# Kernel optimization log

Measured on AMD Instinct MI355X. Metric: run time of the kernel, lower is better.

Reference implementation:

```python
import jax, jax.numpy as jnp
import numpy as np

N_EMBD = 1024
N_HEADS = 16
HEAD_DIM = N_EMBD // N_HEADS


def setup_inputs() -> dict:
    key = jax.random.key(0)
    ks = jax.random.split(key, 5)
    s = 0.02
    return {
        "x": jax.random.normal(ks[0], (4, 2048, N_EMBD), dtype=jnp.float32),
        "w_attn": jax.random.normal(ks[1], (N_EMBD, 3 * N_EMBD), dtype=jnp.float32) * s,
        "b_attn": jnp.zeros((3 * N_EMBD,), dtype=jnp.float32),
        "w_proj": jax.random.normal(ks[2], (N_EMBD, N_EMBD), dtype=jnp.float32) * s,
        "b_proj": jnp.zeros((N_EMBD,), dtype=jnp.float32),
    }


def reference(x, w_attn, b_attn, w_proj, b_proj):
    B, T, C = x.shape
    H, D = N_HEADS, HEAD_DIM
    qkv = x @ w_attn + b_attn                      # [B,T,3C]
    q, k, v = jnp.split(qkv, 3, axis=-1)
    q = q.reshape(B, T, H, D).transpose(0, 2, 1, 3)  # [B,H,T,D]
    k = k.reshape(B, T, H, D).transpose(0, 2, 1, 3)
    v = v.reshape(B, T, H, D).transpose(0, 2, 1, 3)
    # Faithful to source bug: divide by d**(-0.5) == multiply by sqrt(d)
    scale = jnp.asarray(D, x.dtype) ** 0.5
    scores = jnp.einsum("bhqd,bhkd->bhqk", q, k) * scale  # [B,H,T,T]
    causal = jnp.tril(jnp.ones((T, T), dtype=bool))
    scores = jnp.where(causal[None, None], scores, -jnp.inf)
    attn = jax.nn.softmax(scores, axis=-1)
    y = jnp.einsum("bhqk,bhkd->bhqd", attn, v)     # [B,H,T,D]
    y = y.transpose(0, 2, 1, 3).reshape(B, T, C)
    return y @ w_proj + b_proj
```

## Files before the change

### kernel.cpp

```cpp
#include <hip/hip_runtime.h>
#include <cmath>

#define BB 4
#define TT 2048
#define CC 1024
#define HH 16
#define DD 64
#define MM (BB*TT)

typedef _Float16 f16x8 __attribute__((ext_vector_type(8)));
typedef _Float16 f16x4 __attribute__((ext_vector_type(4)));
typedef _Float16 f16x2 __attribute__((ext_vector_type(2)));
typedef float f32x4 __attribute__((ext_vector_type(4)));
typedef unsigned short ushort_t;

#define MFMA16(a,b,c) __builtin_amdgcn_mfma_f32_16x16x16f16(a,b,c,0,0,0)

__device__ __forceinline__ unsigned short f2h(float f) {
    _Float16 h = (_Float16)f;
    return __builtin_bit_cast(unsigned short, h);
}

__device__ __forceinline__ f16x2 cvt_pk(float a, float b) {
    return __builtin_bit_cast(f16x2, __builtin_amdgcn_cvt_pkrtz(a, b));
}

__device__ __forceinline__ void gld16(const void* gsrc, void* ldst) {
    void* g = const_cast<void*>(gsrc);
    __builtin_amdgcn_global_load_lds(
        (__attribute__((address_space(1))) void*)g,
        (__attribute__((address_space(3))) void*)ldst,
        16, 0, 0);
}

__global__ __launch_bounds__(256)
void cvt4_kernel(const float* __restrict__ in, ushort_t* __restrict__ out, long n4) {
    long i = (long)blockIdx.x * blockDim.x + threadIdx.x;
    if (i >= n4) return;
    float4 v = ((const float4*)in)[i];
    ushort4 o;
    o.x = f2h(v.x); o.y = f2h(v.y); o.z = f2h(v.z); o.w = f2h(v.w);
    ((ushort4*)out)[i] = o;
}

__global__ __launch_bounds__(256)
void trcvt_kernel(const float* __restrict__ in, ushort_t* __restrict__ out,
                  int K, int N) {
    __shared__ float T[32][33];
    const int tx = threadIdx.x & 31;
    const int ty = threadIdx.x >> 5;
    const int n0 = blockIdx.x * 32;
    const int k0 = blockIdx.y * 32;
    #pragma unroll
    for (int i = 0; i < 4; ++i)
        T[ty + i * 8][tx] = in[(size_t)(k0 + ty + i * 8) * N + n0 + tx];
    __syncthreads();
    #pragma unroll
    for (int i = 0; i < 4; ++i)
        out[(size_t)(n0 + ty + i * 8) * K + k0 + tx] = f2h(T[tx][ty + i * 8]);
}

template<int N, bool QKV>
__global__ __launch_bounds__(256)
void hgemm_kernel(const ushort_t* __restrict__ A, const ushort_t* __restrict__ Bt,
                  const float* __restrict__ bias, float* __restrict__ out,
                  ushort_t* __restrict__ qh, ushort_t* __restrict__ kh,
                  ushort_t* __restrict__ vh)
{
    const int K = 1024;
    __shared__ ushort_t As[128 * 32];
    __shared__ ushort_t Bs[128 * 32];

    const int tid  = threadIdx.x;
    const int lane = tid & 63;
    const int wave = tid >> 6;
    const int wm   = (wave & 1) * 64;
    const int wn   = (wave >> 1) * 64;
    const int m0   = blockIdx.y * 128;
    const int n0   = blockIdx.x * 128;
    const int lrow = lane & 15;
    const int quad = lane >> 4;

    const int u0 = wave * 64 + lane;
    const int u1 = u0 + 256;
    const size_t gA0 = (size_t)(m0 + (u0 >> 2)) * K + (u0 & 3) * 8;
    const size_t gA1 = (size_t)(m0 + (u1 >> 2)) * K + (u1 & 3) * 8;
    const size_t gB0 = (size_t)(n0 + (u0 >> 2)) * K + (u0 & 3) * 8;
    const size_t gB1 = (size_t)(n0 + (u1 >> 2)) * K + (u1 & 3) * 8;
    ushort_t* ldsA0 = &As[(wave * 64) * 8];
    ushort_t* ldsA1 = &As[(256 + wave * 64) * 8];
    ushort_t* ldsB0 = &Bs[(wave * 64) * 8];
    ushort_t* ldsB1 = &Bs[(256 + wave * 64) * 8];

    f32x4 acc[4][4];
    const f32x4 z = {0.f, 0.f, 0.f, 0.f};
    #pragma unroll
    for (int mt = 0; mt < 4; ++mt)
        #pragma unroll
        for (int nt = 0; nt < 4; ++nt)
            acc[mt][nt] = z;

    for (int kk = 0; kk < K; kk += 32) {
        gld16(&A[gA0 + kk],  ldsA0);
        gld16(&A[gA1 + kk],  ldsA1);
        gld16(&Bt[gB0 + kk], ldsB0);
        gld16(&Bt[gB1 + kk], ldsB1);
        __syncthreads();

        f16x8 af[4], bf[4];
        #pragma unroll
        for (int mt = 0; mt < 4; ++mt)
            af[mt] = *(const f16x8*)&As[(wm + mt * 16 + lrow) * 32 + quad * 8];
        #pragma unroll
        for (int nt = 0; nt < 4; ++nt)
            bf[nt] = *(const f16x8*)&Bs[(wn + nt * 16 + lrow) * 32 + quad * 8];
        #pragma unroll
        for (int mt = 0; mt < 4; ++mt)
            #pragma unroll
            for (int nt = 0; nt < 4; ++nt)
                acc[mt][nt] = __builtin_amdgcn_mfma_f32_16x16x32_f16(
                    af[mt], bf[nt], acc[mt][nt], 0, 0, 0);
        __syncthreads();
    }

    #pragma unroll
    for (int mt = 0; mt < 4; ++mt) {
        const int rbase = m0 + wm + mt * 16 + quad * 4;
        #pragma unroll
        for (int nt = 0; nt < 4; ++nt) {
            const int col = n0 + wn + nt * 16 + lrow;
            const float bv = bias[col];
            if (QKV) {
                const int which = col >> 10;
                const int c = col & 1023;
                const int h = c >> 6, d = c & 63;
                const int b = rbase >> 11, t0 = rbase & 2047;
                if (which == 2) {
                    ushort4 pk;
                    pk.x = f2h(acc[mt][nt][0] + bv);
                    pk.y = f2h(acc[mt][nt][1] + bv);
                    pk.z = f2h(acc[mt][nt][2] + bv);
                    pk.w = f2h(acc[mt][nt][3] + bv);
                    *(ushort4*)&vh[(((size_t)b * HH + h) * DD + d) * TT + t0] = pk;
                } else {
                    ushort_t* dst = which ? kh : qh;
                    const float sc = which ? 1.0f : 8.0f * 1.44269504088896f;
                    #pragma unroll
                    for (int r = 0; r < 4; ++r)
                        dst[(((size_t)b * HH + h) * TT + t0 + r) * DD + d] =
                            f2h((acc[mt][nt][r] + bv) * sc);
                }
            } else {
                #pragma unroll
                for (int r = 0; r < 4; ++r)
                    out[(size_t)(rbase + r) * N + col] = acc[mt][nt][r] + bv;
            }
        }
    }
}

__global__ __launch_bounds__(256, 4)
void attn_mfma_kernel(const ushort_t* __restrict__ qh, const ushort_t* __restrict__ kh,
                      const ushort_t* __restrict__ vh, ushort_t* __restrict__ yh)
{
    __shared__ ushort_t Ks[2][64 * 72];
    __shared__ ushort_t Vs[2][64 * 72];

    const int pr   = blockIdx.x;
    const int bh   = blockIdx.y;
    const int qtA  = 31 - pr;
    const int qtB  = pr;
    const int tid  = threadIdx.x;
    const int lane = tid & 63;
    const int w    = tid >> 6;
    const int lrow = lane & 15;
    const int quad = lane >> 4;

    const ushort_t* qbase = qh + (size_t)bh * TT * DD;
    const ushort_t* kbase = kh + (size_t)bh * TT * DD;
    const ushort_t* vbase = vh + (size_t)bh * DD * TT;
    const int b = bh >> 4, h = bh & 15;

    const int ur = tid >> 3;
    const int uc = (tid & 7) * 8;

    int q0w = qtA * 64 + w * 16;
    f16x8 aq0 = *(const f16x8*)&qbase[(size_t)(q0w + lrow) * DD + quad * 8];
    f16x8 aq1 = *(const f16x8*)&qbase[(size_t)(q0w + lrow) * DD + 32 + quad * 8];

    const f32x4 z = {0.f, 0.f, 0.f, 0.f};
    f32x4 o[4] = {z, z, z, z};
    float mi = -1e30f, li = 0.f;

    uint4 kr0 = *(const uint4*)&kbase[(size_t)ur * DD + uc];
    uint4 kr1 = *(const uint4*)&kbase[(size_t)(ur + 32) * DD + uc];
    uint4 vr0 = *(const uint4*)&vbase[(size_t)ur * TT + uc];
    uint4 vr1 = *(const uint4*)&vbase[(size_t)(ur + 32) * TT + uc];

    *(uint4*)&Ks[0][(ur)      * 72 + uc] = kr0;
    *(uint4*)&Ks[0][(ur + 32) * 72 + uc] = kr1;
    *(uint4*)&Vs[0][(ur)      * 72 + uc] = vr0;
    *(uint4*)&Vs[0][(ur + 32) * 72 + uc] = vr1;
    {
        const int nkt = (1 <= qtA) ? 1 : 0;
        const int nb  = nkt * 64;
        kr0 = *(const uint4*)&kbase[(size_t)(nb + ur) * DD + uc];
        kr1 = *(const uint4*)&kbase[(size_t)(nb + ur + 32) * DD + uc];
        vr0 = *(const uint4*)&vbase[(size_t)ur * TT + nb + uc];
        vr1 = *(const uint4*)&vbase[(size_t)(ur + 32) * TT + nb + uc];
    }
    __syncthreads();

    for (int i = 0; i <= 32; ++i) {
        const int cur = i & 1;
        if (i == qtA + 1) {
            #pragma unroll
            for (int r = 0; r < 4; ++r) {
                const float inv = 1.0f / __shfl(li, quad * 4 + r, 64);
                const int t = q0w + quad * 4 + r;
                #pragma unroll
                for (int dt = 0; dt < 4; ++dt)
                    yh[((size_t)b * TT + t) * CC + h * 64 + dt * 16 + lrow] =
                        f2h(o[dt][r] * inv);
            }
            q0w = qtB * 64 + w * 16;
            aq0 = *(const f16x8*)&qbase[(size_t)(q0w + lrow) * DD + quad * 8];
            aq1 = *(const f16x8*)&qbase[(size_t)(q0w + lrow) * DD + 32 + quad * 8];
            #pragma unroll
            for (int dt = 0; dt < 4; ++dt) o[dt] = z;
            mi = -1e30f; li = 0.f;
        }
        const int kt = (i <= qtA) ? i : i - qtA - 1;

        f32x4 sv[4];
        __builtin_amdgcn_s_setprio(1);
        #pragma unroll
        for (int c = 0; c < 4; ++c) {
            f16x8 ka = *(const f16x8*)&Ks[cur][(c * 16 + lrow) * 72 + quad * 8];
            f16x8 kb = *(const f16x8*)&Ks[cur][(c * 16 + lrow) * 72 + 32 + quad * 8];
            sv[c] = __builtin_amdgcn_mfma_f32_16x16x32_f16(ka, aq0, z, 0, 0, 0);
            sv[c] = __builtin_amdgcn_mfma_f32_16x16x32_f16(kb, aq1, sv[c], 0, 0, 0);
        }
        __builtin_amdgcn_s_setprio(0);

        const int kt2 = kt * 64;
        const int qg  = q0w + lrow;
        const bool diag = (i == qtA) || (i == 32);
        if (diag) {
            #pragma unroll
            for (int c = 0; c < 4; ++c)
                #pragma unroll
                for (int r = 0; r < 4; ++r)
                    if (kt2 + c * 16 + quad * 4 + r > qg) sv[c][r] = -3e38f;
        }
        float mc[4];
        #pragma unroll
        for (int c = 0; c < 4; ++c)
            mc[c] = fmaxf(fmaxf(sv[c][0], sv[c][1]), fmaxf(sv[c][2], sv[c][3]));
        float m = fmaxf(fmaxf(mc[0], mc[1]), fmaxf(mc[2], mc[3]));
        m = fmaxf(m, __shfl_xor(m, 16, 64));
        m = fmaxf(m, __shfl_xor(m, 32, 64));

        if (__any(m > mi + 8.0f)) {
            const float mnew  = fmaxf(mi, m);
            const float alpha = exp2f(mi - mnew);
            mi = mnew;
            li *= alpha;
            #pragma unroll
            for (int r = 0; r < 4; ++r) {
                const float ar = __shfl(alpha, quad * 4 + r, 64);
                #pragma unroll
                for (int dt = 0; dt < 4; ++dt) o[dt][r] *= ar;
            }
        }

        f16x4 ap[4];
        float rc[4];
        #pragma unroll
        for (int c = 0; c < 4; ++c) {
            const float p0 = exp2f(sv[c][0] - mi);
            const float p1 = exp2f(sv[c][1] - mi);
            const float p2 = exp2f(sv[c][2] - mi);
            const float p3 = exp2f(sv[c][3] - mi);
            rc[c] = (p0 + p1) + (p2 + p3);
            const f16x2 lo = cvt_pk(p0, p1);
            const f16x2 hi = cvt_pk(p2, p3);
            ap[c][0] = lo[0]; ap[c][1] = lo[1]; ap[c][2] = hi[0]; ap[c][3] = hi[1];
        }
        float rs = (rc[0] + rc[1]) + (rc[2] + rc[3]);
        rs += __shfl_xor(rs, 16, 64);
        rs += __shfl_xor(rs, 32, 64);
        li += rs;

        __builtin_amdgcn_s_setprio(1);
        #pragma unroll
        for (int dt = 0; dt < 4; ++dt)
            #pragma unroll
            for (int c = 0; c < 4; ++c) {
                f16x4 vb = *(const f16x4*)&Vs[cur][(dt * 16 + lrow) * 72 + c * 16 + quad * 4];
                o[dt] = MFMA16(ap[c], vb, o[dt]);
            }
        __builtin_amdgcn_s_setprio(0);

        if (i < 32) {
            const int nxt = cur ^ 1;
            *(uint4*)&Ks[nxt][(ur)      * 72 + uc] = kr0;
            *(uint4*)&Ks[nxt][(ur + 32) * 72 + uc] = kr1;
            *(uint4*)&Vs[nxt][(ur)      * 72 + uc] = vr0;
            *(uint4*)&Vs[nxt][(ur + 32) * 72 + uc] = vr1;
            if (i < 31) {
                const int ni  = i + 2;
                const int nkt = (ni <= qtA) ? ni : ni - qtA - 1;
                const int nb  = nkt * 64;
                kr0 = *(const uint4*)&kbase[(size_t)(nb + ur) * DD + uc];
                kr1 = *(const uint4*)&kbase[(size_t)(nb + ur + 32) * DD + uc];
                vr0 = *(const uint4*)&vbase[(size_t)ur * TT + nb + uc];
                vr1 = *(const uint4*)&vbase[(size_t)(ur + 32) * TT + nb + uc];
            }
        }
        __syncthreads();
    }

    #pragma unroll
    for (int r = 0; r < 4; ++r) {
        const float inv = 1.0f / __shfl(li, quad * 4 + r, 64);
        const int t = q0w + quad * 4 + r;
        #pragma unroll
        for (int dt = 0; dt < 4; ++dt)
            yh[((size_t)b * TT + t) * CC + h * 64 + dt * 16 + lrow] =
                f2h(o[dt][r] * inv);
    }
}

extern "C" void kernel_launch(void* const* d_in, const int* in_sizes, int n_in,
                              void* d_out, int out_size, void* d_ws, size_t ws_size,
                              hipStream_t stream) {
    const float* x      = (const float*)d_in[0];
    const float* w_attn = (const float*)d_in[1];
    const float* b_attn = (const float*)d_in[2];
    const float* w_proj = (const float*)d_in[3];
    const float* b_proj = (const float*)d_in[4];
    float* out = (float*)d_out;

    const size_t per = (size_t)BB * HH * TT * DD;
    ushort_t* qh  = (ushort_t*)d_ws;
    ushort_t* kh  = qh + per;
    ushort_t* vh  = kh + per;
    ushort_t* xh  = vh + per;
    ushort_t* yh  = xh;
    ushort_t* wat = xh + (size_t)MM * CC;
    ushort_t* wpt = wat + (size_t)3 * CC * CC;

    cvt4_kernel<<<(MM * CC / 4 + 255) / 256, 256, 0, stream>>>(x, xh, MM * CC / 4);
    trcvt_kernel<<<dim3(3 * CC / 32, CC / 32), 256, 0, stream>>>(w_attn, wat, CC, 3 * CC);
    trcvt_kernel<<<dim3(CC / 32, CC / 32), 256, 0, stream>>>(w_proj, wpt, CC, CC);

    hgemm_kernel<3 * CC, true><<<dim3(3 * CC / 128, MM / 128), 256, 0, stream>>>(
        xh, wat, b_attn, nullptr, qh, kh, vh);

    attn_mfma_kernel<<<dim3(16, BB * HH), 256, 0, stream>>>(qh, kh, vh, yh);

    hgemm_kernel<CC, false><<<dim3(CC / 128, MM / 128), 256, 0, stream>>>(
        yh, wpt, b_proj, out, nullptr, nullptr, nullptr);
}
```

Before: 283.8 us.

## Rewrite GEMMs with 4-slot LDS pipeline, larger tiles and swizzled layout

Replaces the single-buffered 128x128 GEMM with a 512-thread kernel using 256-wide N tiles (256 or 128 M), a 4-slot LDS ring buffer with prefetch two k-steps ahead, and a single barrier per iteration. It also XOR-swizzles LDS addresses to reduce bank conflicts and raises wave priority around the MFMA block. The intent is to hide global load latency and improve data reuse in both the QKV and output projections. The cost is more LDS per block (up to 128KB), which limits occupancy, and correctness now depends on hand-tuned vmcnt waits.

```diff
diff --git a/kernel.cpp b/kernel.cpp
--- a/kernel.cpp
+++ b/kernel.cpp
@@ -60,75 +60,102 @@
         out[(size_t)(n0 + ty + i * 8) * K + k0 + tx] = f2h(T[tx][ty + i * 8]);
 }
 
-template<int N, bool QKV>
-__global__ __launch_bounds__(256)
-void hgemm_kernel(const ushort_t* __restrict__ A, const ushort_t* __restrict__ Bt,
-                  const float* __restrict__ bias, float* __restrict__ out,
-                  ushort_t* __restrict__ qh, ushort_t* __restrict__ kh,
-                  ushort_t* __restrict__ vh)
+template<int BM, int NN, bool QKV>
+__global__ __launch_bounds__(512, 2)
+void hgemm2_kernel(const ushort_t* __restrict__ A, const ushort_t* __restrict__ Bt,
+                   const float* __restrict__ bias, float* __restrict__ out,
+                   ushort_t* __restrict__ qh, ushort_t* __restrict__ kh,
+                   ushort_t* __restrict__ vh)
 {
-    const int K = 1024;
-    __shared__ ushort_t As[128 * 32];
-    __shared__ ushort_t Bs[128 * 32];
+    constexpr int K    = 1024;
+    constexpr int MT   = BM / 32;
+    constexpr int AJ   = BM / 128;
+    constexpr int AH   = BM * 32;
+    constexpr int BH   = 256 * 32;
+    constexpr int SLOT = AH + BH;
+    extern __shared__ ushort_t LDS[];
 
     const int tid  = threadIdx.x;
     const int lane = tid & 63;
-    const int wave = tid >> 6;
-    const int wm   = (wave & 1) * 64;
-    const int wn   = (wave >> 1) * 64;
-    const int m0   = blockIdx.y * 128;
-    const int n0   = blockIdx.x * 128;
+    const int wid  = tid >> 6;
+    const int wm   = wid >> 2;
+    const int wn   = wid & 3;
     const int lrow = lane & 15;
     const int quad = lane >> 4;
-
-    const int u0 = wave * 64 + lane;
-    const int u1 = u0 + 256;
-    const size_t gA0 = (size_t)(m0 + (u0 >> 2)) * K + (u0 & 3) * 8;
-    const size_t gA1 = (size_t)(m0 + (u1 >> 2)) * K + (u1 & 3) * 8;
-    const size_t gB0 = (size_t)(n0 + (u0 >> 2)) * K + (u0 & 3) * 8;
-    const size_t gB1 = (size_t)(n0 + (u1 >> 2)) * K + (u1 & 3) * 8;
-    ushort_t* ldsA0 = &As[(wave * 64) * 8];
-    ushort_t* ldsA1 = &As[(256 + wave * 64) * 8];
-    ushort_t* ldsB0 = &Bs[(wave * 64) * 8];
-    ushort_t* ldsB1 = &Bs[(256 + wave * 64) * 8];
-
-    f32x4 acc[4][4];
+    const int m0   = blockIdx.y * BM;
+    const int n0   = blockIdx.x * 256;
+
+    const int lsw   = (lane * 16) ^ ((lane & 32) ? 32 : 0);
+    const int rowin = lsw >> 6;
+    const int scolh = (lsw & 63) >> 1;
+    unsigned voffA[AJ], voffB[2];
+    #pragma unroll
+    for (int j = 0; j < AJ; ++j)
+        voffA[j] = (unsigned)(m0 + (j * 8 + wid) * 16 + rowin) * K + scolh;
+    #pragma unroll
+    for (int j = 0; j < 2; ++j)
+        voffB[j] = (unsigned)(n0 + (j * 8 + wid) * 16 + rowin) * K + scolh;
+    const int ldsW = wid * 512;
+    const int rdo = (lrow * 32 + quad * 8) ^ ((lrow & 8) ? 16 : 0);
+
+    f32x4 acc[MT][4];
     const f32x4 z = {0.f, 0.f, 0.f, 0.f};
     #pragma unroll
-    for (int mt = 0; mt < 4; ++mt)
+    for (int mt = 0; mt < MT; ++mt)
         #pragma unroll
         for (int nt = 0; nt < 4; ++nt)
             acc[mt][nt] = z;
 
-    for (int kk = 0; kk < K; kk += 32) {
-        gld16(&A[gA0 + kk],  ldsA0);
-        gld16(&A[gA1 + kk],  ldsA1);
-        gld16(&Bt[gB0 + kk], ldsB0);
-        gld16(&Bt[gB1 + kk], ldsB1);
-        __syncthreads();
-
-        f16x8 af[4], bf[4];
-        #pragma unroll
-        for (int mt = 0; mt < 4; ++mt)
-            af[mt] = *(const f16x8*)&As[(wm + mt * 16 + lrow) * 32 + quad * 8];
+    auto STAGE = [&](int kt) {
+        ushort_t* sb = &LDS[(kt & 3) * SLOT];
+        #pragma unroll
+        for (int j = 0; j < AJ; ++j)
+            gld16(A + voffA[j] + kt * 32, sb + j * 4096 + ldsW);
+        #pragma unroll
+        for (int j = 0; j < 2; ++j)
+            gld16(Bt + voffB[j] + kt * 32, sb + AH + j * 4096 + ldsW);
+    };
+    auto COMPUTE = [&](int kt) {
+        const ushort_t* As = &LDS[(kt & 3) * SLOT];
+        const ushort_t* Bs = As + AH;
+        f16x8 af[MT], bf[4];
+        #pragma unroll
+        for (int mt = 0; mt < MT; ++mt)
+            af[mt] = *(const f16x8*)&As[(wm * MT + mt) * 512 + rdo];
         #pragma unroll
         for (int nt = 0; nt < 4; ++nt)
-            bf[nt] = *(const f16x8*)&Bs[(wn + nt * 16 + lrow) * 32 + quad * 8];
-        #pragma unroll
-        for (int mt = 0; mt < 4; ++mt)
+            bf[nt] = *(const f16x8*)&Bs[(wn * 4 + nt) * 512 + rdo];
+        __builtin_amdgcn_s_setprio(1);
+        #pragma unroll
+        for (int mt = 0; mt < MT; ++mt)
             #pragma unroll
             for (int nt = 0; nt < 4; ++nt)
                 acc[mt][nt] = __builtin_amdgcn_mfma_f32_16x16x32_f16(
                     af[mt], bf[nt], acc[mt][nt], 0, 0, 0);
-        __syncthreads();
-    }
-
-    #pragma unroll
-    for (int mt = 0; mt < 4; ++mt) {
-        const int rbase = m0 + wm + mt * 16 + quad * 4;
+        __builtin_amdgcn_s_setprio(0);
+    };
+
+    STAGE(0);
+    STAGE(1);
+    for (int kt = 0; kt < 31; ++kt) {
+        if constexpr (BM == 256)
+            asm volatile("s_waitcnt vmcnt(4)" ::: "memory");
+        else
+            asm volatile("s_waitcnt vmcnt(3)" ::: "memory");
+        __builtin_amdgcn_s_barrier();
+        if (kt < 30) STAGE(kt + 2);
+        COMPUTE(kt);
+    }
+    asm volatile("s_waitcnt vmcnt(0)" ::: "memory");
+    __builtin_amdgcn_s_barrier();
+    COMPUTE(31);
+
+    #pragma unroll
+    for (int mt = 0; mt < MT; ++mt) {
+        const int rbase = m0 + wm * (BM / 2) + mt * 16 + quad * 4;
         #pragma unroll
         for (int nt = 0; nt < 4; ++nt) {
-            const int col = n0 + wn + nt * 16 + lrow;
+            const int col = n0 + wn * 64 + nt * 16 + lrow;
             const float bv = bias[col];
             if (QKV) {
                 const int which = col >> 10;
@@ -153,7 +180,7 @@
             } else {
                 #pragma unroll
                 for (int r = 0; r < 4; ++r)
-                    out[(size_t)(rbase + r) * N + col] = acc[mt][nt][r] + bv;
+                    out[(size_t)(rbase + r) * NN + col] = acc[mt][nt][r] + bv;
             }
         }
     }
@@ -355,11 +382,13 @@
     trcvt_kernel<<<dim3(3 * CC / 32, CC / 32), 256, 0, stream>>>(w_attn, wat, CC, 3 * CC);
     trcvt_kernel<<<dim3(CC / 32, CC / 32), 256, 0, stream>>>(w_proj, wpt, CC, CC);
 
-    hgemm_kernel<3 * CC, true><<<dim3(3 * CC / 128, MM / 128), 256, 0, stream>>>(
+    hgemm2_kernel<256, 3 * CC, true>
+        <<<dim3(3 * CC / 256, MM / 256), 512, 4 * (256 * 32 + 256 * 32) * 2, stream>>>(
         xh, wat, b_attn, nullptr, qh, kh, vh);
 
     attn_mfma_kernel<<<dim3(16, BB * HH), 256, 0, stream>>>(qh, kh, vh, yh);
 
-    hgemm_kernel<CC, false><<<dim3(CC / 128, MM / 128), 256, 0, stream>>>(
+    hgemm2_kernel<128, CC, false>
+        <<<dim3(CC / 256, MM / 128), 512, 4 * (128 * 32 + 256 * 32) * 2, stream>>>(
         yh, wpt, b_proj, out, nullptr, nullptr, nullptr);
 }
```

Result: no change. 280.1 us (-1.3%).
